# Kernel optimization log

Hardware: AMD Instinct MI355X
Metric: run time of the kernel (lower is better)

## Reference

```python
import jax, jax.numpy as jnp
import numpy as np

N_NODES = 100000
N_EDGES = 2048
L_TOK = 8
HID = 64
D_IN = L_TOK * HID      # 512, flattened token embeddings per node/edge
D_GNN = 128             # GNN output dim; reshaped to seq_len=2 of HID
VOCAB = 32000
FFN = 256


def setup_inputs() -> dict:
    key = jax.random.key(0)
    ks = jax.random.split(key, 14)
    s = 0.02  # weight scale for numerical stability
    return {
        'node_tokens': jax.random.randint(ks[0], (N_NODES, L_TOK), 0, VOCAB, dtype=jnp.int32),
        'edge_tokens': jax.random.randint(ks[1], (N_EDGES, L_TOK), 0, VOCAB, dtype=jnp.int32),
        'edge_index': jax.random.randint(ks[2], (2, N_EDGES), 0, N_NODES, dtype=jnp.int32),
        'embed_table': jax.random.normal(ks[3], (VOCAB, HID), jnp.float32) * s,
        'W_self': jax.random.normal(ks[4], (D_IN, D_GNN), jnp.float32) * s,
        'W_nbr': jax.random.normal(ks[5], (D_IN, D_GNN), jnp.float32) * s,
        'Wq': jax.random.normal(ks[6], (HID, HID), jnp.float32) * s,
        'Wk': jax.random.normal(ks[7], (HID, HID), jnp.float32) * s,
        'Wv': jax.random.normal(ks[8], (HID, HID), jnp.float32) * s,
        'Wo': jax.random.normal(ks[9], (HID, HID), jnp.float32) * s,
        'W1': jax.random.normal(ks[10], (HID, FFN), jnp.float32) * s,
        'W2': jax.random.normal(ks[11], (FFN, HID), jnp.float32) * s,
        'lm_W': jax.random.normal(ks[12], (HID, VOCAB), jnp.float32) * s,
        'lm_b': jnp.zeros((VOCAB,), jnp.float32),
    }


def _ln(x):
    m = jnp.mean(x, axis=-1, keepdims=True)
    v = jnp.var(x, axis=-1, keepdims=True)
    return (x - m) / jnp.sqrt(v + 1e-5)


def reference(node_tokens, edge_tokens, edge_index, embed_table, W_self, W_nbr,
              Wq, Wk, Wv, Wo, W1, W2, lm_W, lm_b):
    n_nodes = node_tokens.shape[0]
    n_edges = edge_tokens.shape[0]
    # per-batch embedding lookups, flattened per node/edge: [N, L*H], [E, L*H]
    node_emb = embed_table[node_tokens].reshape(n_nodes, -1)
    edge_emb = embed_table[edge_tokens].reshape(n_edges, -1)
    src, dst = edge_index[0], edge_index[1]
    # GNN message passing: gather source node feats + edge feats, scatter-add at dst
    msg = (node_emb[src] + edge_emb) @ W_nbr                  # [E, D_GNN]
    agg = jax.ops.segment_sum(msg, dst, num_segments=n_nodes)  # [N, D_GNN]
    h = jax.nn.relu(node_emb @ W_self + agg)                   # [N, D_GNN]
    # edge feature gather-sum: embeddings[idx0] + embeddings[idx1]
    edge_h = h[src] + h[dst]                                   # [E, D_GNN]
    x = edge_h.reshape(n_edges, -1, HID)                       # [E, S=2, H]
    # transformer block (self-attention + FFN)
    q, k, v = x @ Wq, x @ Wk, x @ Wv
    scores = jnp.einsum('bsh,bth->bst', q, k) / jnp.sqrt(jnp.float32(HID))
    a = jnp.einsum('bst,bth->bsh', jax.nn.softmax(scores, axis=-1), v) @ Wo
    x = _ln(x + a)
    x = _ln(x + jax.nn.relu(x @ W1) @ W2)
    # lm head + softmax
    logits = x @ lm_W + lm_b                                   # [E, S, V]
    probs = jax.nn.softmax(logits, axis=-1)
    # mask_label on edge tokens: only (deterministic) row 0, non-special tokens kept
    special = (edge_tokens[..., None] == jnp.arange(4, dtype=edge_tokens.dtype)).any(-1)
    mask_row = jnp.zeros((n_edges,), bool).at[0].set(True)
    masked = mask_row[:, None] & (~special)
    labels = jnp.where(masked, edge_tokens, -100)
    return (labels, probs)
```

## Files before the change

kernel.cpp:

```cpp
#include <hip/hip_runtime.h>

#define NE 2048
#define VOC 32000

typedef __attribute__((ext_vector_type(8))) short short8;
typedef __attribute__((ext_vector_type(4))) float f32x4;

#define OFF_LMWT   0u
#define OFF_WNBRT  4096000u
#define OFF_WSELFT 4227072u
#define OFF_AALL   4358144u
#define OFF_MSG    10649600u
#define OFF_XS     11698176u
#define OFF_XD     12746752u
#define OFF_XB     13795328u
#define OFF_RSUMS  14319616u

__device__ __forceinline__ short f2bf(float f) {
  union { float f; unsigned u; } c; c.f = f;
  unsigned r = (c.u + 0x7FFFu + ((c.u >> 16) & 1u)) >> 16;
  return (short)r;
}

__device__ __forceinline__ float wave_sum64(float v) {
#pragma unroll
  for (int m = 1; m < 64; m <<= 1) v += __shfl_xor(v, m, 64);
  return v;
}

__global__ __launch_bounds__(256) void k0_prep(
    const float* __restrict__ lm_W, const float* __restrict__ W_nbr,
    const float* __restrict__ W_self, const int* __restrict__ edge_tokens,
    short* __restrict__ lm_Wt, short* __restrict__ Wnbrt,
    short* __restrict__ Wselft, float* __restrict__ rsums,
    float* __restrict__ out_labels) {
  int b = blockIdx.x, t = threadIdx.x;
  if (b == 532) {
    for (int i = t; i < 4096; i += 256) rsums[i] = 0.f;
    return;
  }
  if (b >= 533) {
    int base = (b - 533) * 1024 + t;
#pragma unroll
    for (int it = 0; it < 4; ++it) {
      int i = base + it * 256;
      int e = i >> 3;
      int tok = edge_tokens[i];
      float val = -100.f;
      if (e == 0 && tok >= 4) val = (float)tok;
      out_labels[i] = val;
    }
    return;
  }
  const float* src; short* dst; int R, C, tb;
  if (b < 500)      { src = lm_W;   dst = lm_Wt;  R = 64;  C = VOC; tb = b; }
  else if (b < 516) { src = W_nbr;  dst = Wnbrt;  R = 512; C = 128; tb = b - 500; }
  else              { src = W_self; dst = Wselft; R = 512; C = 128; tb = b - 516; }
  __shared__ float tile[64][65];
  int tiles_c = C >> 6;
  int r0 = (tb / tiles_c) << 6;
  int c0 = (tb % tiles_c) << 6;
  int lr = t >> 6, lc = t & 63;
#pragma unroll
  for (int rr = 0; rr < 16; ++rr) {
    int r = rr * 4 + lr;
    tile[r][lc] = src[(r0 + r) * C + c0 + lc];
  }
  __syncthreads();
#pragma unroll
  for (int rr = 0; rr < 16; ++rr) {
    int cc = rr * 4 + lr;
    dst[(c0 + cc) * R + r0 + lc] = f2bf(tile[lc][cc]);
  }
}

__global__ __launch_bounds__(256) void k1a_gather(
    const int* __restrict__ node_tokens, const int* __restrict__ edge_tokens,
    const int* __restrict__ edge_index, const float* __restrict__ embed,
    short* __restrict__ A_all) {
  int t = blockIdx.x * 256 + threadIdx.x;
  int row = t >> 6;
  int rem = t & 63;
  int j = rem >> 3;
  int h0 = (rem & 7) << 3;
  int kind = row >> 11;
  int e = row & 2047;
  int n = (kind == 2) ? edge_index[NE + e] : edge_index[e];
  int tok = node_tokens[n * 8 + j];
  const float* ep = embed + tok * 64 + h0;
  f32x4 a0 = *(const f32x4*)ep;
  f32x4 a1 = *(const f32x4*)(ep + 4);
  if (kind == 0) {
    int etok = edge_tokens[e * 8 + j];
    const float* ep2 = embed + etok * 64 + h0;
    a0 += *(const f32x4*)ep2;
    a1 += *(const f32x4*)(ep2 + 4);
  }
  short8 ov;
#pragma unroll
  for (int i = 0; i < 4; ++i) { ov[i] = f2bf(a0[i]); ov[4 + i] = f2bf(a1[i]); }
  *(short8*)(A_all + row * 512 + j * 64 + h0) = ov;
}

__global__ __launch_bounds__(256) void k1b_gemm(
    const short* __restrict__ A_all, const short* __restrict__ Wnbrt,
    const short* __restrict__ Wselft, float* __restrict__ msg,
    float* __restrict__ xsarr, float* __restrict__ xdarr) {
  int t = threadIdx.x;
  int w = t >> 6, l = t & 63;
  int lm = l & 15, lq = l >> 4;
  int r0 = blockIdx.x * 32;
  int kind = r0 >> 11;
  const short* B = (kind == 0) ? Wnbrt : Wselft;
  float* outp = (kind == 0) ? msg : (kind == 1) ? xsarr : xdarr;
  int orow0 = r0 & 2047;
  f32x4 acc[2][2] = {};
  for (int ks = 0; ks < 16; ++ks) {
    int kk = ks * 32 + lq * 8;
    short8 a0 = *(const short8*)(A_all + (r0 + lm) * 512 + kk);
    short8 a1 = *(const short8*)(A_all + (r0 + 16 + lm) * 512 + kk);
    short8 b0 = *(const short8*)(B + (w * 32 + lm) * 512 + kk);
    short8 b1 = *(const short8*)(B + (w * 32 + 16 + lm) * 512 + kk);
    acc[0][0] = __builtin_amdgcn_mfma_f32_16x16x32_bf16(a0, b0, acc[0][0], 0, 0, 0);
    acc[0][1] = __builtin_amdgcn_mfma_f32_16x16x32_bf16(a0, b1, acc[0][1], 0, 0, 0);
    acc[1][0] = __builtin_amdgcn_mfma_f32_16x16x32_bf16(a1, b0, acc[1][0], 0, 0, 0);
    acc[1][1] = __builtin_amdgcn_mfma_f32_16x16x32_bf16(a1, b1, acc[1][1], 0, 0, 0);
  }
#pragma unroll
  for (int mf = 0; mf < 2; ++mf)
#pragma unroll
    for (int nf = 0; nf < 2; ++nf)
#pragma unroll
      for (int r = 0; r < 4; ++r) {
        int m = orow0 + mf * 16 + lq * 4 + r;
        int n = w * 32 + nf * 16 + lm;
        outp[m * 128 + n] = acc[mf][nf][r];
      }
}

__global__ __launch_bounds__(128) void k23_fused(
    const int* __restrict__ edge_index, const float* __restrict__ msg,
    const float* __restrict__ xsarr, const float* __restrict__ xdarr,
    const float* __restrict__ Wq, const float* __restrict__ Wk,
    const float* __restrict__ Wv, const float* __restrict__ Wo,
    const float* __restrict__ W1, const float* __restrict__ W2,
    short* __restrict__ Xb) {
  int e = blockIdx.x, t = threadIdx.x;
  int s = t >> 6, h = t & 63;
  __shared__ __align__(16) float xlds[2][64];
  __shared__ float klds[2][64];
  __shared__ float vlds[2][64];
  __shared__ __align__(16) float alds[2][64];
  __shared__ __align__(16) float h1[2][256];
  __shared__ int lst[2][128];
  __shared__ int lcnt[2];

  int srcu = edge_index[e], dstu = edge_index[NE + e];
  float acc_s = 0.f, acc_d = 0.f;
  for (int c = 0; c < 16; ++c) {
    if (t < 2) lcnt[t] = 0;
    __syncthreads();
    int ep = c * 128 + t;
    int d = edge_index[NE + ep];
    if (d == srcu) { int p = atomicAdd(&lcnt[0], 1); lst[0][p] = ep; }
    if (d == dstu) { int p = atomicAdd(&lcnt[1], 1); lst[1][p] = ep; }
    __syncthreads();
    int c0 = lcnt[0], c1 = lcnt[1];
    for (int i = 0; i < c0; ++i) acc_s += msg[lst[0][i] * 128 + t];
    for (int i = 0; i < c1; ++i) acc_d += msg[lst[1][i] * 128 + t];
    __syncthreads();
  }
  float hs = fmaxf(xsarr[e * 128 + t] + acc_s, 0.f);
  float hd = fmaxf(xdarr[e * 128 + t] + acc_d, 0.f);
  float xv = hs + hd;
  ((float*)xlds)[t] = xv;
  __syncthreads();

  float q = 0.f, kk = 0.f, vv = 0.f;
  for (int k4 = 0; k4 < 64; k4 += 4) {
    f32x4 xr = *(const f32x4*)&xlds[s][k4];
#pragma unroll
    for (int i = 0; i < 4; ++i) {
      int kidx = k4 + i;
      q  += xr[i] * Wq[kidx * 64 + h];
      kk += xr[i] * Wk[kidx * 64 + h];
      vv += xr[i] * Wv[kidx * 64 + h];
    }
  }
  klds[s][h] = kk;
  vlds[s][h] = vv;
  __syncthreads();
  float sc0 = wave_sum64(q * klds[0][h]) * 0.125f;
  float sc1 = wave_sum64(q * klds[1][h]) * 0.125f;
  float mx = fmaxf(sc0, sc1);
  float e0 = __expf(sc0 - mx), e1 = __expf(sc1 - mx);
  float pin = 1.f / (e0 + e1);
  float av = (e0 * pin) * vlds[0][h] + (e1 * pin) * vlds[1][h];
  alds[s][h] = av;
  __syncthreads();
  float o = 0.f;
  for (int k4 = 0; k4 < 64; k4 += 4) {
    f32x4 ar = *(const f32x4*)&alds[s][k4];
#pragma unroll
    for (int i = 0; i < 4; ++i) o += ar[i] * Wo[(k4 + i) * 64 + h];
  }
  float xa = xv + o;
  float mean = wave_sum64(xa) * (1.f / 64.f);
  float var = wave_sum64(xa * xa) * (1.f / 64.f) - mean * mean;
  float x1 = (xa - mean) * rsqrtf(var + 1e-5f);
  __syncthreads();
  ((float*)xlds)[t] = x1;
  __syncthreads();
  f32x4 hh = {0.f, 0.f, 0.f, 0.f};
  int f0 = h * 4;
  for (int k4 = 0; k4 < 64; k4 += 4) {
    f32x4 xr = *(const f32x4*)&xlds[s][k4];
#pragma unroll
    for (int i = 0; i < 4; ++i) {
      f32x4 wrow = *(const f32x4*)&W1[(k4 + i) * 256 + f0];
#pragma unroll
      for (int jj = 0; jj < 4; ++jj) hh[jj] += xr[i] * wrow[jj];
    }
  }
#pragma unroll
  for (int jj = 0; jj < 4; ++jj) hh[jj] = fmaxf(hh[jj], 0.f);
  *(f32x4*)&h1[s][f0] = hh;
  __syncthreads();
  float o2 = 0.f;
  for (int f4 = 0; f4 < 256; f4 += 4) {
    f32x4 hr = *(const f32x4*)&h1[s][f4];
#pragma unroll
    for (int i = 0; i < 4; ++i) o2 += hr[i] * W2[(f4 + i) * 64 + h];
  }
  float xb2 = x1 + o2;
  float mean2 = wave_sum64(xb2) * (1.f / 64.f);
  float var2 = wave_sum64(xb2 * xb2) * (1.f / 64.f) - mean2 * mean2;
  float x2 = (xb2 - mean2) * rsqrtf(var2 + 1e-5f);
  Xb[(e * 2 + s) * 64 + h] = f2bf(x2);
}

__global__ __launch_bounds__(256) void d1_sums(
    const short* __restrict__ Xb, const short* __restrict__ lm_Wt,
    const float* __restrict__ lm_b, float* __restrict__ rsums) {
  int t = threadIdx.x;
  int w = t >> 6, l = t & 63;
  int lm = l & 15, lq = l >> 4;
  int b = blockIdx.x;
  int x = b & 7, j = b >> 3;
  int slice = x * 2 + (j & 1);
  int mb0 = (j >> 1) * 64;
  short8 af[4][2];
#pragma unroll
  for (int mf = 0; mf < 4; ++mf)
#pragma unroll
    for (int ks = 0; ks < 2; ++ks)
      af[mf][ks] = *(const short8*)(Xb + (mb0 + mf * 16 + lm) * 64 + ks * 32 + lq * 8);
  float sums[4][4] = {};
  for (int vt = 0; vt < 8; ++vt) {
    int tile = slice * 8 + vt;
    if (tile >= 125) break;
    int n0 = tile * 256 + w * 64;
    short8 bf[4][2];
#pragma unroll
    for (int nf = 0; nf < 4; ++nf)
#pragma unroll
      for (int ks = 0; ks < 2; ++ks)
        bf[nf][ks] = *(const short8*)(lm_Wt + (n0 + nf * 16 + lm) * 64 + ks * 32 + lq * 8);
    f32x4 acc[4][4] = {};
#pragma unroll
    for (int ks = 0; ks < 2; ++ks)
#pragma unroll
      for (int mf = 0; mf < 4; ++mf)
#pragma unroll
        for (int nf = 0; nf < 4; ++nf)
          acc[mf][nf] = __builtin_amdgcn_mfma_f32_16x16x32_bf16(af[mf][ks], bf[nf][ks], acc[mf][nf], 0, 0, 0);
    float bv[4];
#pragma unroll
    for (int nf = 0; nf < 4; ++nf) bv[nf] = lm_b[n0 + nf * 16 + lm];
#pragma unroll
    for (int mf = 0; mf < 4; ++mf)
#pragma unroll
      for (int nf = 0; nf < 4; ++nf)
#pragma unroll
        for (int r = 0; r < 4; ++r)
          sums[mf][r] += __expf(acc[mf][nf][r] + bv[nf]);
  }
#pragma unroll
  for (int mf = 0; mf < 4; ++mf)
#pragma unroll
    for (int r = 0; r < 4; ++r) {
      float v = sums[mf][r];
      v += __shfl_xor(v, 1, 64);
      v += __shfl_xor(v, 2, 64);
      v += __shfl_xor(v, 4, 64);
      v += __shfl_xor(v, 8, 64);
      sums[mf][r] = v;
    }
  __shared__ float ls[64];
  if (t < 64) ls[t] = 0.f;
  __syncthreads();
  if (lm == 0) {
#pragma unroll
    for (int mf = 0; mf < 4; ++mf)
#pragma unroll
      for (int r = 0; r < 4; ++r)
        atomicAdd(&ls[mf * 16 + lq * 4 + r], sums[mf][r]);
  }
  __syncthreads();
  if (t < 64) atomicAdd(&rsums[mb0 + t], ls[t]);
}

__global__ __launch_bounds__(256) void d2_probs(
    const short* __restrict__ Xb, const short* __restrict__ lm_Wt,
    const float* __restrict__ lm_b, const float* __restrict__ rsums,
    float* __restrict__ out_probs) {
  int t = threadIdx.x;
  int w = t >> 6, l = t & 63;
  int lm = l & 15, lq = l >> 4;
  int b = blockIdx.x;
  int x = b & 7, j = b >> 3;
  int tile = x * 16 + (j & 15);
  if (tile >= 125) return;
  int mb0 = (j >> 4) * 64;
  int n0 = tile * 256 + w * 64;
  __shared__ float invs[64];
  if (t < 64) invs[t] = 1.f / rsums[mb0 + t];
  __syncthreads();
  short8 xf[4][2], wf[4][2];
#pragma unroll
  for (int mf = 0; mf < 4; ++mf)
#pragma unroll
    for (int ks = 0; ks < 2; ++ks)
      xf[mf][ks] = *(const short8*)(Xb + (mb0 + mf * 16 + lm) * 64 + ks * 32 + lq * 8);
#pragma unroll
  for (int nf = 0; nf < 4; ++nf)
#pragma unroll
    for (int ks = 0; ks < 2; ++ks)
      wf[nf][ks] = *(const short8*)(lm_Wt + (n0 + nf * 16 + lm) * 64 + ks * 32 + lq * 8);
  f32x4 acc[4][4] = {};
#pragma unroll
  for (int ks = 0; ks < 2; ++ks)
#pragma unroll
    for (int mf = 0; mf < 4; ++mf)
#pragma unroll
      for (int nf = 0; nf < 4; ++nf)
        acc[mf][nf] = __builtin_amdgcn_mfma_f32_16x16x32_bf16(wf[nf][ks], xf[mf][ks], acc[mf][nf], 0, 0, 0);
  f32x4 bq[4];
#pragma unroll
  for (int nf = 0; nf < 4; ++nf)
    bq[nf] = *(const f32x4*)(lm_b + n0 + nf * 16 + lq * 4);
#pragma unroll
  for (int mf = 0; mf < 4; ++mf) {
    float iv = invs[mf * 16 + lm];
    size_t rowbase = (size_t)(mb0 + mf * 16 + lm) * VOC;
#pragma unroll
    for (int nf = 0; nf < 4; ++nf) {
      f32x4 p;
#pragma unroll
      for (int r = 0; r < 4; ++r)
        p[r] = __expf(acc[mf][nf][r] + bq[nf][r]) * iv;
      __builtin_nontemporal_store(p, (f32x4*)(out_probs + rowbase + n0 + nf * 16 + lq * 4));
    }
  }
}

extern "C" void kernel_launch(void* const* d_in, const int* in_sizes, int n_in,
                              void* d_out, int out_size, void* d_ws, size_t ws_size,
                              hipStream_t stream) {
  const int* node_tokens = (const int*)d_in[0];
  const int* edge_tokens = (const int*)d_in[1];
  const int* edge_index  = (const int*)d_in[2];
  const float* embed     = (const float*)d_in[3];
  const float* W_self    = (const float*)d_in[4];
  const float* W_nbr     = (const float*)d_in[5];
  const float* Wq        = (const float*)d_in[6];
  const float* Wk        = (const float*)d_in[7];
  const float* Wv        = (const float*)d_in[8];
  const float* Wo        = (const float*)d_in[9];
  const float* W1        = (const float*)d_in[10];
  const float* W2        = (const float*)d_in[11];
  const float* lm_W      = (const float*)d_in[12];
  const float* lm_b      = (const float*)d_in[13];

  char* ws = (char*)d_ws;
  short* lm_Wt  = (short*)(ws + OFF_LMWT);
  short* Wnbrt  = (short*)(ws + OFF_WNBRT);
  short* Wselft = (short*)(ws + OFF_WSELFT);
  short* A_all  = (short*)(ws + OFF_AALL);
  float* msg    = (float*)(ws + OFF_MSG);
  float* xsarr  = (float*)(ws + OFF_XS);
  float* xdarr  = (float*)(ws + OFF_XD);
  short* Xb     = (short*)(ws + OFF_XB);
  float* rsums  = (float*)(ws + OFF_RSUMS);
  float* out    = (float*)d_out;

  k0_prep<<<549, 256, 0, stream>>>(lm_W, W_nbr, W_self, edge_tokens,
                                   lm_Wt, Wnbrt, Wselft, rsums, out);
  k1a_gather<<<1536, 256, 0, stream>>>(node_tokens, edge_tokens, edge_index,
                                       embed, A_all);
  k1b_gemm<<<192, 256, 0, stream>>>(A_all, Wnbrt, Wselft, msg, xsarr, xdarr);
  k23_fused<<<2048, 128, 0, stream>>>(edge_index, msg, xsarr, xdarr,
                                      Wq, Wk, Wv, Wo, W1, W2, Xb);
  d1_sums<<<1024, 256, 0, stream>>>(Xb, lm_Wt, lm_b, rsums);
  d2_probs<<<8192, 256, 0, stream>>>(Xb, lm_Wt, lm_b, rsums, out + 16384);
}
```

Measured before the change: 714.9 us.

## Retile LM-head kernels to keep vocab weights resident and loop over row groups

Both LM-head kernels now assign each block one 256-column vocab tile and 256 rows (four 64-row groups). The weight and bias fragments are loaded once and reused across the row groups, replacing the old scheme where d2 loaded a fresh weight tile per block and d1 looped over vocab tiles. This cuts the block count to 2000 with no idle blocks, and d1 now issues one global atomic per row group per tile. The aim is less weight reloading and launch overhead. The cost is more global atomics on rsums and extra syncthreads per loop iteration.

```diff
diff --git a/kernel.cpp b/kernel.cpp
--- a/kernel.cpp
+++ b/kernel.cpp
@@ -245,27 +245,27 @@
   int t = threadIdx.x;
   int w = t >> 6, l = t & 63;
   int lm = l & 15, lq = l >> 4;
-  int b = blockIdx.x;
-  int x = b & 7, j = b >> 3;
-  int slice = x * 2 + (j & 1);
-  int mb0 = (j >> 1) * 64;
-  short8 af[4][2];
-#pragma unroll
-  for (int mf = 0; mf < 4; ++mf)
+  int tile = blockIdx.x >> 4;
+  int rs = blockIdx.x & 15;
+  int n0 = tile * 256 + w * 64;
+  short8 bf[4][2];
+#pragma unroll
+  for (int nf = 0; nf < 4; ++nf)
 #pragma unroll
     for (int ks = 0; ks < 2; ++ks)
-      af[mf][ks] = *(const short8*)(Xb + (mb0 + mf * 16 + lm) * 64 + ks * 32 + lq * 8);
-  float sums[4][4] = {};
-  for (int vt = 0; vt < 8; ++vt) {
-    int tile = slice * 8 + vt;
-    if (tile >= 125) break;
-    int n0 = tile * 256 + w * 64;
-    short8 bf[4][2];
-#pragma unroll
-    for (int nf = 0; nf < 4; ++nf)
+      bf[nf][ks] = *(const short8*)(lm_Wt + (n0 + nf * 16 + lm) * 64 + ks * 32 + lq * 8);
+  float bv[4];
+#pragma unroll
+  for (int nf = 0; nf < 4; ++nf) bv[nf] = lm_b[n0 + nf * 16 + lm];
+  __shared__ float ls[4][64];
+  for (int rg = 0; rg < 4; ++rg) {
+    int mb0 = rs * 256 + rg * 64;
+    short8 af[4][2];
+#pragma unroll
+    for (int mf = 0; mf < 4; ++mf)
 #pragma unroll
       for (int ks = 0; ks < 2; ++ks)
-        bf[nf][ks] = *(const short8*)(lm_Wt + (n0 + nf * 16 + lm) * 64 + ks * 32 + lq * 8);
+        af[mf][ks] = *(const short8*)(Xb + (mb0 + mf * 16 + lm) * 64 + ks * 32 + lq * 8);
     f32x4 acc[4][4] = {};
 #pragma unroll
     for (int ks = 0; ks < 2; ++ks)
@@ -274,40 +274,23 @@
 #pragma unroll
         for (int nf = 0; nf < 4; ++nf)
           acc[mf][nf] = __builtin_amdgcn_mfma_f32_16x16x32_bf16(af[mf][ks], bf[nf][ks], acc[mf][nf], 0, 0, 0);
-    float bv[4];
-#pragma unroll
-    for (int nf = 0; nf < 4; ++nf) bv[nf] = lm_b[n0 + nf * 16 + lm];
 #pragma unroll
     for (int mf = 0; mf < 4; ++mf)
 #pragma unroll
-      for (int nf = 0; nf < 4; ++nf)
-#pragma unroll
-        for (int r = 0; r < 4; ++r)
-          sums[mf][r] += __expf(acc[mf][nf][r] + bv[nf]);
-  }
-#pragma unroll
-  for (int mf = 0; mf < 4; ++mf)
-#pragma unroll
-    for (int r = 0; r < 4; ++r) {
-      float v = sums[mf][r];
-      v += __shfl_xor(v, 1, 64);
-      v += __shfl_xor(v, 2, 64);
-      v += __shfl_xor(v, 4, 64);
-      v += __shfl_xor(v, 8, 64);
-      sums[mf][r] = v;
-    }
-  __shared__ float ls[64];
-  if (t < 64) ls[t] = 0.f;
-  __syncthreads();
-  if (lm == 0) {
-#pragma unroll
-    for (int mf = 0; mf < 4; ++mf)
-#pragma unroll
-      for (int r = 0; r < 4; ++r)
-        atomicAdd(&ls[mf * 16 + lq * 4 + r], sums[mf][r]);
-  }
-  __syncthreads();
-  if (t < 64) atomicAdd(&rsums[mb0 + t], ls[t]);
+      for (int r = 0; r < 4; ++r) {
+        float s = 0.f;
+#pragma unroll
+        for (int nf = 0; nf < 4; ++nf) s += __expf(acc[mf][nf][r] + bv[nf]);
+        s += __shfl_xor(s, 1, 64);
+        s += __shfl_xor(s, 2, 64);
+        s += __shfl_xor(s, 4, 64);
+        s += __shfl_xor(s, 8, 64);
+        if (lm == 0) ls[w][mf * 16 + lq * 4 + r] = s;
+      }
+    __syncthreads();
+    if (t < 64) atomicAdd(&rsums[mb0 + t], ls[0][t] + ls[1][t] + ls[2][t] + ls[3][t]);
+    __syncthreads();
+  }
 }
 
 __global__ __launch_bounds__(256) void d2_probs(
@@ -317,49 +300,49 @@
   int t = threadIdx.x;
   int w = t >> 6, l = t & 63;
   int lm = l & 15, lq = l >> 4;
-  int b = blockIdx.x;
-  int x = b & 7, j = b >> 3;
-  int tile = x * 16 + (j & 15);
-  if (tile >= 125) return;
-  int mb0 = (j >> 4) * 64;
+  int tile = blockIdx.x >> 4;
+  int rs = blockIdx.x & 15;
   int n0 = tile * 256 + w * 64;
-  __shared__ float invs[64];
-  if (t < 64) invs[t] = 1.f / rsums[mb0 + t];
-  __syncthreads();
-  short8 xf[4][2], wf[4][2];
-#pragma unroll
-  for (int mf = 0; mf < 4; ++mf)
-#pragma unroll
-    for (int ks = 0; ks < 2; ++ks)
-      xf[mf][ks] = *(const short8*)(Xb + (mb0 + mf * 16 + lm) * 64 + ks * 32 + lq * 8);
+  short8 wf[4][2];
 #pragma unroll
   for (int nf = 0; nf < 4; ++nf)
 #pragma unroll
     for (int ks = 0; ks < 2; ++ks)
       wf[nf][ks] = *(const short8*)(lm_Wt + (n0 + nf * 16 + lm) * 64 + ks * 32 + lq * 8);
-  f32x4 acc[4][4] = {};
-#pragma unroll
-  for (int ks = 0; ks < 2; ++ks)
-#pragma unroll
-    for (int mf = 0; mf < 4; ++mf)
-#pragma unroll
-      for (int nf = 0; nf < 4; ++nf)
-        acc[mf][nf] = __builtin_amdgcn_mfma_f32_16x16x32_bf16(wf[nf][ks], xf[mf][ks], acc[mf][nf], 0, 0, 0);
   f32x4 bq[4];
 #pragma unroll
   for (int nf = 0; nf < 4; ++nf)
     bq[nf] = *(const f32x4*)(lm_b + n0 + nf * 16 + lq * 4);
-#pragma unroll
-  for (int mf = 0; mf < 4; ++mf) {
-    float iv = invs[mf * 16 + lm];
-    size_t rowbase = (size_t)(mb0 + mf * 16 + lm) * VOC;
-#pragma unroll
-    for (int nf = 0; nf < 4; ++nf) {
-      f32x4 p;
-#pragma unroll
-      for (int r = 0; r < 4; ++r)
-        p[r] = __expf(acc[mf][nf][r] + bq[nf][r]) * iv;
-      __builtin_nontemporal_store(p, (f32x4*)(out_probs + rowbase + n0 + nf * 16 + lq * 4));
+  for (int rg = 0; rg < 4; ++rg) {
+    int mb0 = rs * 256 + rg * 64;
+    short8 xf[4][2];
+#pragma unroll
+    for (int mf = 0; mf < 4; ++mf)
+#pragma unroll
+      for (int ks = 0; ks < 2; ++ks)
+        xf[mf][ks] = *(const short8*)(Xb + (mb0 + mf * 16 + lm) * 64 + ks * 32 + lq * 8);
+    float iv[4];
+#pragma unroll
+    for (int mf = 0; mf < 4; ++mf) iv[mf] = 1.f / rsums[mb0 + mf * 16 + lm];
+    f32x4 acc[4][4] = {};
+#pragma unroll
+    for (int ks = 0; ks < 2; ++ks)
+#pragma unroll
+      for (int mf = 0; mf < 4; ++mf)
+#pragma unroll
+        for (int nf = 0; nf < 4; ++nf)
+          acc[mf][nf] = __builtin_amdgcn_mfma_f32_16x16x32_bf16(wf[nf][ks], xf[mf][ks], acc[mf][nf], 0, 0, 0);
+#pragma unroll
+    for (int mf = 0; mf < 4; ++mf) {
+      size_t rowbase = (size_t)(mb0 + mf * 16 + lm) * VOC;
+#pragma unroll
+      for (int nf = 0; nf < 4; ++nf) {
+        f32x4 p;
+#pragma unroll
+        for (int r = 0; r < 4; ++r)
+          p[r] = __expf(acc[mf][nf][r] + bq[nf][r]) * iv[mf];
+        __builtin_nontemporal_store(p, (f32x4*)(out_probs + rowbase + n0 + nf * 16 + lq * 4));
+      }
     }
   }
 }
@@ -401,6 +384,6 @@
   k1b_gemm<<<192, 256, 0, stream>>>(A_all, Wnbrt, Wselft, msg, xsarr, xdarr);
   k23_fused<<<2048, 128, 0, stream>>>(edge_index, msg, xsarr, xdarr,
                                       Wq, Wk, Wv, Wo, W1, W2, Xb);
-  d1_sums<<<1024, 256, 0, stream>>>(Xb, lm_Wt, lm_b, rsums);
-  d2_probs<<<8192, 256, 0, stream>>>(Xb, lm_Wt, lm_b, rsums, out + 16384);
-}
+  d1_sums<<<2000, 256, 0, stream>>>(Xb, lm_Wt, lm_b, rsums);
+  d2_probs<<<2000, 256, 0, stream>>>(Xb, lm_Wt, lm_b, rsums, out + 16384);
+}
```

Result: slower. 754.9 us (+5.6%).
